# Optimization experiments

Hardware: AMD Instinct MI355X
Metric: run time of the kernel (lower is better)

The kernel has to match this reference:

```python
import jax, jax.numpy as jnp
import numpy as np

C = 256          # channels
H = 8            # attn heads
DH = C // H      # head dim
G = 2048         # number of graphs
NPG = 100        # nodes per graph
N = G * NPG      # total nodes
EPS = 1e-5       # batchnorm eps


def setup_inputs() -> dict:
    key = jax.random.key(0)
    ks = jax.random.split(key, 14)
    std = 0.02
    inp = {
        "x0": jax.random.normal(ks[0], (N, C), jnp.float32),
        "x1": jax.random.normal(ks[1], (N, C), jnp.float32),
        "batch": jnp.repeat(jnp.arange(G, dtype=jnp.int64), NPG)[:, None],
        # branch 0: linear + BN affine
        "p0_W": jax.random.normal(ks[2], (C, C), jnp.float32) * std,
        "p0_b": jnp.zeros((C,), jnp.float32),
        "p0_g": jnp.ones((C,), jnp.float32),
        "p0_beta": jnp.zeros((C,), jnp.float32),
        # branch 1
        "p1_W": jax.random.normal(ks[3], (C, C), jnp.float32) * std,
        "p1_b": jnp.zeros((C,), jnp.float32),
        "p1_g": jnp.ones((C,), jnp.float32),
        "p1_beta": jnp.zeros((C,), jnp.float32),
        # merge
        "merge_W": jax.random.normal(ks[4], (C, 2 * C), jnp.float32) * std,
        "merge_b": jnp.zeros((C,), jnp.float32),
        # MHA in_proj (packed q,k,v as in torch) and out_proj
        "in_proj_W": jax.random.normal(ks[5], (3 * C, C), jnp.float32) * std,
        "in_proj_b": jnp.zeros((3 * C,), jnp.float32),
        "out_proj_W": jax.random.normal(ks[6], (C, C), jnp.float32) * std,
        "out_proj_b": jnp.zeros((C,), jnp.float32),
        # readout
        "readout_W": jax.random.normal(ks[7], (1, C), jnp.float32) * std,
        "readout_b": jnp.zeros((1,), jnp.float32),
    }
    return inp


def _lin_bn_relu(x, W, b, g, beta):
    y = x @ W.T + b
    mu = jnp.mean(y, axis=0)
    var = jnp.var(y, axis=0)  # biased, matches torch BN training normalization
    return jax.nn.relu((y - mu) * jax.lax.rsqrt(var + EPS) * g + beta)


def reference(x0, x1, batch,
              p0_W, p0_b, p0_g, p0_beta,
              p1_W, p1_b, p1_g, p1_beta,
              merge_W, merge_b,
              in_proj_W, in_proj_b,
              out_proj_W, out_proj_b,
              readout_W, readout_b):
    seg = batch[:, 0]                                   # [N] sorted graph ids
    h0 = _lin_bn_relu(x0, p0_W, p0_b, p0_g, p0_beta)
    h1 = _lin_bn_relu(x1, p1_W, p1_b, p1_g, p1_beta)
    x = jnp.concatenate([h0, h1], axis=1) @ merge_W.T + merge_b  # [N,C]

    Wq, Wk, Wv = jnp.split(in_proj_W, 3, axis=0)
    bq, bk, bv = jnp.split(in_proj_b, 3, axis=0)
    # query is all-ones (length-1 sequence), shared across graphs
    q = (jnp.ones((C,), x.dtype) @ Wq.T + bq).reshape(H, DH) / jnp.sqrt(jnp.float32(DH))
    k = (x @ Wk.T + bk).reshape(-1, H, DH)              # [N,H,dh]
    v = (x @ Wv.T + bv).reshape(-1, H, DH)              # [N,H,dh]

    scores = jnp.einsum('hd,nhd->nh', q, k)            # [N,H]
    # segmented softmax over nodes of each graph
    m = jax.ops.segment_max(scores, seg, num_segments=G)      # [G,H]
    e = jnp.exp(scores - m[seg])                               # [N,H]
    denom = jax.ops.segment_sum(e, seg, num_segments=G)       # [G,H]
    pooled = jax.ops.segment_sum(e[:, :, None] * v, seg, num_segments=G)  # [G,H,dh]
    pooled = pooled / denom[:, :, None]

    attn = pooled.reshape(G, C) @ out_proj_W.T + out_proj_b   # [G,C]
    out = jnp.tanh(attn @ readout_W.T + readout_b)            # [G,1]
    return out
```

## Files before the change

kernel.cpp:

```cpp
#include <hip/hip_runtime.h>
#include <stdint.h>

#define NROWS 204800
#define NBLK_Y 1600
#define GRP 2048
#define NPG 100

typedef __attribute__((ext_vector_type(4))) float f32x4;
typedef __attribute__((ext_vector_type(8))) short bf16x8;
typedef __attribute__((ext_vector_type(4))) short bf16x4;

__device__ __forceinline__ unsigned bcu(float f){ union{float f;unsigned u;}c; c.f=f; return c.u; }
__device__ __forceinline__ float bcf(unsigned u){ union{unsigned u;float f;}c; c.u=u; return c.f; }
__device__ __forceinline__ short f2bf_rne(float f){ unsigned u=bcu(f); unsigned r=(u+0x7fffu+((u>>16)&1u))>>16; return (short)r; }
__device__ __forceinline__ unsigned pk_trunc(float lo, float hi){
  return __builtin_amdgcn_perm(bcu(hi), bcu(lo), 0x07060302u);
}
__device__ __forceinline__ f32x4 mfma16(bf16x8 a, bf16x8 b, f32x4 c){
  return __builtin_amdgcn_mfma_f32_16x16x32_bf16(a, b, c, 0, 0, 0);
}
#define BFLY16(v) { v += __shfl_xor(v,1); v += __shfl_xor(v,2); v += __shfl_xor(v,4); v += __shfl_xor(v,8); }

__global__ void k_cast_w(const float* __restrict__ w0, const float* __restrict__ w1,
                         short* __restrict__ out){
  int t = blockIdx.x*256 + threadIdx.x;
  const float* src = (t < 16384) ? w0 : w1;
  int base = (t & 16383) * 4;
  f32x4 v = *(const f32x4*)(src + base);
  bf16x4 o; o[0]=f2bf_rne(v[0]); o[1]=f2bf_rne(v[1]); o[2]=f2bf_rne(v[2]); o[3]=f2bf_rne(v[3]);
  *(bf16x4*)(out + ((t<16384)?0:65536) + base) = o;
}

__global__ void __launch_bounds__(256, 2)
k_gemm_y(const float* __restrict__ x0, const float* __restrict__ x1,
         const short* __restrict__ Wb,
         const float* __restrict__ b0p, const float* __restrict__ b1p,
         short* __restrict__ y0, short* __restrict__ y1,
         float* __restrict__ stats){
  __shared__ float st_sh[4][256][2];
  int bid = blockIdx.x;
  int which = (bid >= NBLK_Y) ? 1 : 0;
  const float* __restrict__ X = which ? x1 : x0;
  short* __restrict__ Y = which ? y1 : y0;
  const short* __restrict__ W = Wb + which*65536;
  const float* __restrict__ bias = which ? b1p : b0p;
  int n0 = (which ? bid - NBLK_Y : bid) * 128;
  int t = threadIdx.x, lane = t & 63, w = t >> 6;
  int l15 = lane & 15, q = lane >> 4;

  f32x4 acc[16][2];
  #pragma unroll
  for (int mt=0; mt<16; mt++){ acc[mt][0] = f32x4{0,0,0,0}; acc[mt][1] = f32x4{0,0,0,0}; }

  int nb = n0 + w*32;
  const float* xr0 = X + (nb + l15)*256;
  const float* xr1 = X + (nb + 16 + l15)*256;
  const short* wrow = W + l15*256;

  for (int ks=0; ks<8; ks++){
    int kq = ks*32 + q*8;
    f32x4 xa0 = *(const f32x4*)(xr0 + kq);
    f32x4 xb0 = *(const f32x4*)(xr0 + kq + 4);
    f32x4 xa1 = *(const f32x4*)(xr1 + kq);
    f32x4 xb1 = *(const f32x4*)(xr1 + kq + 4);
    int4 p0; p0.x=(int)pk_trunc(xa0[0],xa0[1]); p0.y=(int)pk_trunc(xa0[2],xa0[3]);
             p0.z=(int)pk_trunc(xb0[0],xb0[1]); p0.w=(int)pk_trunc(xb0[2],xb0[3]);
    int4 p1; p1.x=(int)pk_trunc(xa1[0],xa1[1]); p1.y=(int)pk_trunc(xa1[2],xa1[3]);
             p1.z=(int)pk_trunc(xb1[0],xb1[1]); p1.w=(int)pk_trunc(xb1[2],xb1[3]);
    bf16x8 bf0 = __builtin_bit_cast(bf16x8, p0);
    bf16x8 bf1 = __builtin_bit_cast(bf16x8, p1);
    #pragma unroll
    for (int mt=0; mt<16; mt++){
      bf16x8 af = *(const bf16x8*)(wrow + mt*4096 + kq);
      acc[mt][0] = mfma16(af, bf0, acc[mt][0]);
      acc[mt][1] = mfma16(af, bf1, acc[mt][1]);
    }
  }

  short* yo0 = Y + (nb + l15)*256 + q*4;
  short* yo1 = Y + (nb + 16 + l15)*256 + q*4;
  #pragma unroll
  for (int mt=0; mt<16; mt++){
    f32x4 bb = *(const f32x4*)(bias + mt*16 + q*4);
    f32x4 v0 = acc[mt][0] + bb;
    f32x4 v1 = acc[mt][1] + bb;
    int2 s0v; s0v.x=(int)pk_trunc(v0[0],v0[1]); s0v.y=(int)pk_trunc(v0[2],v0[3]);
    *(int2*)(yo0 + mt*16) = s0v;
    int2 s1v; s1v.x=(int)pk_trunc(v1[0],v1[1]); s1v.y=(int)pk_trunc(v1[2],v1[3]);
    *(int2*)(yo1 + mt*16) = s1v;
    float sa0=v0[0]+v1[0], sa1=v0[1]+v1[1], sa2=v0[2]+v1[2], sa3=v0[3]+v1[3];
    float qa0=v0[0]*v0[0]+v1[0]*v1[0], qa1=v0[1]*v0[1]+v1[1]*v1[1];
    float qa2=v0[2]*v0[2]+v1[2]*v1[2], qa3=v0[3]*v0[3]+v1[3]*v1[3];
    BFLY16(sa0); BFLY16(sa1); BFLY16(sa2); BFLY16(sa3);
    BFLY16(qa0); BFLY16(qa1); BFLY16(qa2); BFLY16(qa3);
    if (l15 == 0){
      int c0 = mt*16 + q*4;
      st_sh[w][c0+0][0]=sa0; st_sh[w][c0+0][1]=qa0;
      st_sh[w][c0+1][0]=sa1; st_sh[w][c0+1][1]=qa1;
      st_sh[w][c0+2][0]=sa2; st_sh[w][c0+2][1]=qa2;
      st_sh[w][c0+3][0]=sa3; st_sh[w][c0+3][1]=qa3;
    }
  }
  __syncthreads();
  {
    float ss = st_sh[0][t][0]+st_sh[1][t][0]+st_sh[2][t][0]+st_sh[3][t][0];
    float qq = st_sh[0][t][1]+st_sh[1][t][1]+st_sh[2][t][1]+st_sh[3][t][1];
    int rep = bid & 7;
    atomicAdd(&stats[rep*1024 + which*512 + t], ss);
    atomicAdd(&stats[rep*1024 + which*512 + 256 + t], qq);
  }
}

__global__ void k_small(const float* __restrict__ inW, const float* __restrict__ inB,
                        const float* __restrict__ mergeB,
                        const float* __restrict__ g0, const float* __restrict__ be0,
                        const float* __restrict__ g1, const float* __restrict__ be1,
                        const float* __restrict__ outW, const float* __restrict__ outB,
                        const float* __restrict__ rout, const float* __restrict__ routB,
                        const float* __restrict__ stats,
                        float* __restrict__ prm, float* __restrict__ qk){
  __shared__ float qv_sh[256], ck_sh[256];
  int t = threadIdx.x;
  const float invN = 1.0f/(float)NROWS;
  float s0=0, sq0=0, s1=0, sq1=0;
  for (int r=0;r<8;r++){
    s0  += stats[r*1024 + t];       sq0 += stats[r*1024 + 256 + t];
    s1  += stats[r*1024 + 512 + t]; sq1 += stats[r*1024 + 768 + t];
  }
  {
    float mu = s0*invN, var = sq0*invN - mu*mu;
    float rs = rsqrtf(var + 1e-5f);
    float a = g0[t]*rs;
    prm[t] = a; prm[512+t] = be0[t] - mu*a;
  }
  {
    float mu = s1*invN, var = sq1*invN - mu*mu;
    float rs = rsqrtf(var + 1e-5f);
    float a = g1[t]*rs;
    prm[256+t] = a; prm[768+t] = be1[t] - mu*a;
  }
  float qs = inB[t];
  for (int k=0;k<256;k++) qs += inW[t*256 + k];
  qv_sh[t] = qs * 0.17677669529663689f;
  float cks = inB[256+t];
  for (int m=0;m<256;m++) cks += mergeB[m] * inW[(256+t)*256 + m];
  ck_sh[t] = cks;
  float cvs = inB[512+t];
  for (int m=0;m<256;m++) cvs += mergeB[m] * inW[(512+t)*256 + m];
  prm[1024+t] = cvs;
  float wf = 0;
  for (int m=0;m<256;m++) wf += rout[m] * outW[m*256 + t];
  prm[1288+t] = wf;
  __syncthreads();
  for (int r=0;r<8;r++){
    int idx = r*256 + t; int h = idx>>8, m = idx&255;
    float s = 0;
    for (int d=0;d<32;d++) s += qv_sh[h*32+d] * inW[(256 + h*32 + d)*256 + m];
    qk[h*256+m] = s;
  }
  if (t < 8){
    float cs_ = 0;
    for (int d=0;d<32;d++) cs_ += qv_sh[t*32+d]*ck_sh[t*32+d];
    prm[1280+t] = cs_;
  }
  if (t == 0){
    float cf = routB[0];
    for (int m=0;m<256;m++) cf += rout[m]*outB[m];
    prm[1544] = cf;
  }
}

__global__ void k_wall(const float* __restrict__ inW, const float* __restrict__ mergeW,
                       const float* __restrict__ qk, short* __restrict__ Wall){
  int c = blockIdx.x; int t = threadIdx.x;
  if (c >= 264){
    Wall[c*512 + t] = 0; Wall[c*512 + 256 + t] = 0; return;
  }
  const float* src = (c < 256) ? (inW + (512+c)*256) : (qk + (c-256)*256);
  float a0=0, a1=0;
  for (int m=0;m<256;m++){
    float wm = src[m];
    a0 += wm * mergeW[m*512 + t];
    a1 += wm * mergeW[m*512 + 256 + t];
  }
  Wall[c*512 + t]       = f2bf_rne(a0);
  Wall[c*512 + 256 + t] = f2bf_rne(a1);
}

__global__ void __launch_bounds__(256, 2)
k_fused(const short* __restrict__ y0, const short* __restrict__ y1,
        const short* __restrict__ Wall, const float* __restrict__ prm,
        float* __restrict__ num, float* __restrict__ den){
  __shared__ float a_sh[512], b_sh[512], cv_sh[256], cs_sh[8];
  int t = threadIdx.x, lane = t & 63, w = t >> 6;
  int l15 = lane & 15, q = lane >> 4;
  for (int i=t; i<512; i+=256){ a_sh[i] = prm[i]; b_sh[i] = prm[512+i]; }
  cv_sh[t] = prm[1024+t];
  if (t < 8) cs_sh[t] = prm[1280+t];
  __syncthreads();

  int n0 = blockIdx.x*128, nb = n0 + w*32;
  f32x4 acc[17][2];
  #pragma unroll
  for (int mt=0; mt<17; mt++){ acc[mt][0] = f32x4{0,0,0,0}; acc[mt][1] = f32x4{0,0,0,0}; }

  for (int ks=0; ks<16; ks++){
    int jq = ks*32 + q*8;
    const short* ybase = (ks < 8) ? y0 : y1;
    int jj = jq & 255;
    f32x4 paL = *(const f32x4*)&a_sh[jq];  f32x4 paH = *(const f32x4*)&a_sh[jq+4];
    f32x4 pbL = *(const f32x4*)&b_sh[jq];  f32x4 pbH = *(const f32x4*)&b_sh[jq+4];
    bf16x8 bfr[2];
    #pragma unroll
    for (int nt=0; nt<2; nt++){
      int4 raw = *(const int4*)(ybase + (nb + nt*16 + l15)*256 + jj);
      unsigned r0=(unsigned)raw.x, r1=(unsigned)raw.y, r2=(unsigned)raw.z, r3=(unsigned)raw.w;
      float h0 = fmaxf(fmaf(bcf(r0<<16),         paL[0], pbL[0]), 0.f);
      float h1 = fmaxf(fmaf(bcf(r0&0xffff0000u), paL[1], pbL[1]), 0.f);
      float h2 = fmaxf(fmaf(bcf(r1<<16),         paL[2], pbL[2]), 0.f);
      float h3 = fmaxf(fmaf(bcf(r1&0xffff0000u), paL[3], pbL[3]), 0.f);
      float h4 = fmaxf(fmaf(bcf(r2<<16),         paH[0], pbH[0]), 0.f);
      float h5 = fmaxf(fmaf(bcf(r2&0xffff0000u), paH[1], pbH[1]), 0.f);
      float h6 = fmaxf(fmaf(bcf(r3<<16),         paH[2], pbH[2]), 0.f);
      float h7 = fmaxf(fmaf(bcf(r3&0xffff0000u), paH[3], pbH[3]), 0.f);
      int4 pk; pk.x=(int)pk_trunc(h0,h1); pk.y=(int)pk_trunc(h2,h3);
               pk.z=(int)pk_trunc(h4,h5); pk.w=(int)pk_trunc(h6,h7);
      bfr[nt] = __builtin_bit_cast(bf16x8, pk);
    }
    const short* wbase = Wall + l15*512 + jq;
    #pragma unroll
    for (int mt=0; mt<17; mt++){
      bf16x8 af = *(const bf16x8*)(wbase + mt*8192);
      acc[mt][0] = mfma16(af, bfr[0], acc[mt][0]);
      acc[mt][1] = mfma16(af, bfr[1], acc[mt][1]);
    }
  }

  float e0[4], e1[4];
  #pragma unroll
  for (int i=0;i<4;i++){
    float cadd = (q<2) ? cs_sh[q*4+i] : 0.f;
    e0[i] = (q<2) ? __expf(acc[16][0][i] + cadd) : 0.f;
    e1[i] = (q<2) ? __expf(acc[16][1][i] + cadd) : 0.f;
  }
  #pragma unroll
  for (int nt=0; nt<2; nt++){
    int tb = nb + nt*16;
    int sg = tb/100; int brow = (sg+1)*100 - tb; bool split = brow < 16;
    float d0[4], d1[4];
    #pragma unroll
    for (int i=0;i<4;i++){
      float ev = nt ? e1[i] : e0[i];
      d0[i] = (l15 < brow) ? ev : 0.f; d1[i] = ev - d0[i];
    }
    BFLY16(d0[0]); BFLY16(d0[1]); BFLY16(d0[2]); BFLY16(d0[3]);
    if (split){ BFLY16(d1[0]); BFLY16(d1[1]); BFLY16(d1[2]); BFLY16(d1[3]); }
    if (l15==0 && q<2){
      #pragma unroll
      for (int i=0;i<4;i++) atomicAdd(&den[sg*8 + q*4 + i], d0[i]);
      if (split){
        #pragma unroll
        for (int i=0;i<4;i++) atomicAdd(&den[(sg+1)*8 + q*4 + i], d1[i]);
      }
    }
  }
  #pragma unroll
  for (int mt=0; mt<16; mt++){
    const int h = mt>>1, hq = h>>2, hi = h&3;
    f32x4 cvv = *(const f32x4*)&cv_sh[mt*16 + q*4];
    #pragma unroll
    for (int nt=0; nt<2; nt++){
      float esrc = nt ? e1[hi] : e0[hi];
      float eb = __shfl(esrc, hq*16 + l15, 64);
      int tb = nb + nt*16;
      int sg = tb/100; int brow = (sg+1)*100 - tb; bool split = brow < 16;
      float p0[4], p1[4];
      #pragma unroll
      for (int i=0;i<4;i++){
        float wv = (acc[mt][nt][i] + cvv[i]) * eb;
        p0[i] = (l15 < brow) ? wv : 0.f; p1[i] = wv - p0[i];
      }
      BFLY16(p0[0]); BFLY16(p0[1]); BFLY16(p0[2]); BFLY16(p0[3]);
      if (split){ BFLY16(p1[0]); BFLY16(p1[1]); BFLY16(p1[2]); BFLY16(p1[3]); }
      if (l15==0){
        int c0 = mt*16 + q*4;
        #pragma unroll
        for (int i=0;i<4;i++) atomicAdd(&num[sg*256 + c0 + i], p0[i]);
        if (split){
          #pragma unroll
          for (int i=0;i<4;i++) atomicAdd(&num[(sg+1)*256 + c0 + i], p1[i]);
        }
      }
    }
  }
}

__global__ void k_out(const float* __restrict__ num, const float* __restrict__ den,
                      const float* __restrict__ prm, float* __restrict__ out){
  int g = blockIdx.x; int lane = threadIdx.x;
  f32x4 nm = *(const f32x4*)(num + g*256 + lane*4);
  f32x4 wf = *(const f32x4*)(prm + 1288 + lane*4);
  float dh = den[g*8 + (lane>>3)];
  float v = (nm[0]*wf[0] + nm[1]*wf[1] + nm[2]*wf[2] + nm[3]*wf[3]) / dh;
  v += __shfl_xor(v,1); v += __shfl_xor(v,2); v += __shfl_xor(v,4);
  v += __shfl_xor(v,8); v += __shfl_xor(v,16); v += __shfl_xor(v,32);
  if (lane==0) out[g] = tanhf(v + prm[1544]);
}

extern "C" void kernel_launch(void* const* d_in, const int* in_sizes, int n_in,
                              void* d_out, int out_size, void* d_ws, size_t ws_size,
                              hipStream_t stream){
  const float* x0      = (const float*)d_in[0];
  const float* x1      = (const float*)d_in[1];
  const float* p0_W    = (const float*)d_in[3];
  const float* p0_b    = (const float*)d_in[4];
  const float* p0_g    = (const float*)d_in[5];
  const float* p0_beta = (const float*)d_in[6];
  const float* p1_W    = (const float*)d_in[7];
  const float* p1_b    = (const float*)d_in[8];
  const float* p1_g    = (const float*)d_in[9];
  const float* p1_beta = (const float*)d_in[10];
  const float* merge_W = (const float*)d_in[11];
  const float* merge_b = (const float*)d_in[12];
  const float* inp_W   = (const float*)d_in[13];
  const float* inp_b   = (const float*)d_in[14];
  const float* out_W   = (const float*)d_in[15];
  const float* out_b   = (const float*)d_in[16];
  const float* ro_W    = (const float*)d_in[17];
  const float* ro_b    = (const float*)d_in[18];
  float* outp = (float*)d_out;

  char* ws = (char*)d_ws;
  short* y0w   = (short*)(ws);
  short* y1w   = (short*)(ws + 104857600);
  short* Wb    = (short*)(ws + 209715200);
  short* Wall  = (short*)(ws + 209977344);
  float* stats = (float*)(ws + 210255872);
  float* num   = (float*)(ws + 210288640);
  float* den   = (float*)(ws + 212385792);
  float* prm   = (float*)(ws + 212451328);
  float* qk    = (float*)(ws + 212459520);

  hipMemsetAsync(ws + 210255872, 0, 2195456, stream);

  k_cast_w<<<dim3(128), dim3(256), 0, stream>>>(p0_W, p1_W, Wb);
  k_gemm_y<<<dim3(2*NBLK_Y), dim3(256), 0, stream>>>(x0, x1, Wb, p0_b, p1_b, y0w, y1w, stats);
  k_small<<<dim3(1), dim3(256), 0, stream>>>(inp_W, inp_b, merge_b, p0_g, p0_beta, p1_g, p1_beta,
                                             out_W, out_b, ro_W, ro_b, stats, prm, qk);
  k_wall<<<dim3(272), dim3(256), 0, stream>>>(inp_W, merge_W, qk, Wall);
  k_fused<<<dim3(NBLK_Y), dim3(256), 0, stream>>>(y0w, y1w, Wall, prm, num, den);
  k_out<<<dim3(GRP), dim3(64), 0, stream>>>(num, den, prm, outp);
}
```

Measured before the change: 1.017 ms.

## Restructure GEMMs to keep activations in registers and stream weight tiles per output block

Both the first GEMM and the fused merge/KV kernel now load and convert the whole activation strip into registers up front. They then loop over output column tiles, computing each tile's full K reduction with double-buffered weight fragment loads. This replaces the large per-thread accumulator array with two accumulators, which frees registers; the first kernel's launch bounds are raised to allow 3 blocks per CU. The epilogue work (softmax denominators, weighted num atomics) is interleaved per tile, with the score tile computed first. Register pressure from the held activations and weights may still limit occupancy or cause spills.

```diff
diff --git a/kernel.cpp b/kernel.cpp
--- a/kernel.cpp
+++ b/kernel.cpp
@@ -31,7 +31,7 @@
   *(bf16x4*)(out + ((t<16384)?0:65536) + base) = o;
 }
 
-__global__ void __launch_bounds__(256, 2)
+__global__ void __launch_bounds__(256, 3)
 k_gemm_y(const float* __restrict__ x0, const float* __restrict__ x1,
          const short* __restrict__ Wb,
          const float* __restrict__ b0p, const float* __restrict__ b1p,
@@ -47,43 +47,57 @@
   int n0 = (which ? bid - NBLK_Y : bid) * 128;
   int t = threadIdx.x, lane = t & 63, w = t >> 6;
   int l15 = lane & 15, q = lane >> 4;
-
-  f32x4 acc[16][2];
-  #pragma unroll
-  for (int mt=0; mt<16; mt++){ acc[mt][0] = f32x4{0,0,0,0}; acc[mt][1] = f32x4{0,0,0,0}; }
-
   int nb = n0 + w*32;
-  const float* xr0 = X + (nb + l15)*256;
-  const float* xr1 = X + (nb + 16 + l15)*256;
+
   const short* wrow = W + l15*256;
 
-  for (int ks=0; ks<8; ks++){
-    int kq = ks*32 + q*8;
-    f32x4 xa0 = *(const f32x4*)(xr0 + kq);
-    f32x4 xb0 = *(const f32x4*)(xr0 + kq + 4);
-    f32x4 xa1 = *(const f32x4*)(xr1 + kq);
-    f32x4 xb1 = *(const f32x4*)(xr1 + kq + 4);
-    int4 p0; p0.x=(int)pk_trunc(xa0[0],xa0[1]); p0.y=(int)pk_trunc(xa0[2],xa0[3]);
-             p0.z=(int)pk_trunc(xb0[0],xb0[1]); p0.w=(int)pk_trunc(xb0[2],xb0[3]);
-    int4 p1; p1.x=(int)pk_trunc(xa1[0],xa1[1]); p1.y=(int)pk_trunc(xa1[2],xa1[3]);
-             p1.z=(int)pk_trunc(xb1[0],xb1[1]); p1.w=(int)pk_trunc(xb1[2],xb1[3]);
-    bf16x8 bf0 = __builtin_bit_cast(bf16x8, p0);
-    bf16x8 bf1 = __builtin_bit_cast(bf16x8, p1);
-    #pragma unroll
-    for (int mt=0; mt<16; mt++){
-      bf16x8 af = *(const bf16x8*)(wrow + mt*4096 + kq);
-      acc[mt][0] = mfma16(af, bf0, acc[mt][0]);
-      acc[mt][1] = mfma16(af, bf1, acc[mt][1]);
+  bf16x8 wfA[4], wfB[4];
+  #pragma unroll
+  for (int ks=0; ks<4; ks++)
+    wfA[ks] = *(const bf16x8*)(wrow + ks*32 + q*8);
+
+  bf16x8 xb[2][8];
+  #pragma unroll
+  for (int g=0; g<2; g++){
+    const float* xr = X + (nb + g*16 + l15)*256;
+    #pragma unroll
+    for (int ks=0; ks<8; ks++){
+      int kq = ks*32 + q*8;
+      f32x4 a = *(const f32x4*)(xr + kq);
+      f32x4 b = *(const f32x4*)(xr + kq + 4);
+      int4 p; p.x=(int)pk_trunc(a[0],a[1]); p.y=(int)pk_trunc(a[2],a[3]);
+              p.z=(int)pk_trunc(b[0],b[1]); p.w=(int)pk_trunc(b[2],b[3]);
+      xb[g][ks] = __builtin_bit_cast(bf16x8, p);
     }
   }
 
   short* yo0 = Y + (nb + l15)*256 + q*4;
   short* yo1 = Y + (nb + 16 + l15)*256 + q*4;
+
   #pragma unroll
   for (int mt=0; mt<16; mt++){
+    #pragma unroll
+    for (int ks=0; ks<4; ks++)
+      wfB[ks] = *(const bf16x8*)(wrow + mt*4096 + (ks+4)*32 + q*8);
+    f32x4 acc0 = f32x4{0,0,0,0}, acc1 = f32x4{0,0,0,0};
+    #pragma unroll
+    for (int ks=0; ks<4; ks++){
+      acc0 = mfma16(wfA[ks], xb[0][ks], acc0);
+      acc1 = mfma16(wfA[ks], xb[1][ks], acc1);
+    }
+    if (mt < 15){
+      #pragma unroll
+      for (int ks=0; ks<4; ks++)
+        wfA[ks] = *(const bf16x8*)(wrow + (mt+1)*4096 + ks*32 + q*8);
+    }
+    #pragma unroll
+    for (int ks=0; ks<4; ks++){
+      acc0 = mfma16(wfB[ks], xb[0][ks+4], acc0);
+      acc1 = mfma16(wfB[ks], xb[1][ks+4], acc1);
+    }
     f32x4 bb = *(const f32x4*)(bias + mt*16 + q*4);
-    f32x4 v0 = acc[mt][0] + bb;
-    f32x4 v1 = acc[mt][1] + bb;
+    f32x4 v0 = acc0 + bb;
+    f32x4 v1 = acc1 + bb;
     int2 s0v; s0v.x=(int)pk_trunc(v0[0],v0[1]); s0v.y=(int)pk_trunc(v0[2],v0[3]);
     *(int2*)(yo0 + mt*16) = s0v;
     int2 s1v; s1v.x=(int)pk_trunc(v1[0],v1[1]); s1v.y=(int)pk_trunc(v1[2],v1[3]);
@@ -200,20 +214,24 @@
   __syncthreads();
 
   int n0 = blockIdx.x*128, nb = n0 + w*32;
-  f32x4 acc[17][2];
-  #pragma unroll
-  for (int mt=0; mt<17; mt++){ acc[mt][0] = f32x4{0,0,0,0}; acc[mt][1] = f32x4{0,0,0,0}; }
-
+  const short* wbase = Wall + l15*512;
+
+  bf16x8 wfA[8], wfB[8];
+  #pragma unroll
+  for (int ks=0; ks<8; ks++)
+    wfA[ks] = *(const bf16x8*)(wbase + 16*8192 + ks*32 + q*8);
+
+  bf16x8 xb[2][16];
+  #pragma unroll
   for (int ks=0; ks<16; ks++){
     int jq = ks*32 + q*8;
     const short* ybase = (ks < 8) ? y0 : y1;
     int jj = jq & 255;
     f32x4 paL = *(const f32x4*)&a_sh[jq];  f32x4 paH = *(const f32x4*)&a_sh[jq+4];
     f32x4 pbL = *(const f32x4*)&b_sh[jq];  f32x4 pbH = *(const f32x4*)&b_sh[jq+4];
-    bf16x8 bfr[2];
-    #pragma unroll
-    for (int nt=0; nt<2; nt++){
-      int4 raw = *(const int4*)(ybase + (nb + nt*16 + l15)*256 + jj);
+    #pragma unroll
+    for (int g=0; g<2; g++){
+      int4 raw = *(const int4*)(ybase + (nb + g*16 + l15)*256 + jj);
       unsigned r0=(unsigned)raw.x, r1=(unsigned)raw.y, r2=(unsigned)raw.z, r3=(unsigned)raw.w;
       float h0 = fmaxf(fmaf(bcf(r0<<16),         paL[0], pbL[0]), 0.f);
       float h1 = fmaxf(fmaf(bcf(r0&0xffff0000u), paL[1], pbL[1]), 0.f);
@@ -225,70 +243,89 @@
       float h7 = fmaxf(fmaf(bcf(r3&0xffff0000u), paH[3], pbH[3]), 0.f);
       int4 pk; pk.x=(int)pk_trunc(h0,h1); pk.y=(int)pk_trunc(h2,h3);
                pk.z=(int)pk_trunc(h4,h5); pk.w=(int)pk_trunc(h6,h7);
-      bfr[nt] = __builtin_bit_cast(bf16x8, pk);
-    }
-    const short* wbase = Wall + l15*512 + jq;
-    #pragma unroll
-    for (int mt=0; mt<17; mt++){
-      bf16x8 af = *(const bf16x8*)(wbase + mt*8192);
-      acc[mt][0] = mfma16(af, bfr[0], acc[mt][0]);
-      acc[mt][1] = mfma16(af, bfr[1], acc[mt][1]);
+      xb[g][ks] = __builtin_bit_cast(bf16x8, pk);
     }
   }
 
   float e0[4], e1[4];
-  #pragma unroll
-  for (int i=0;i<4;i++){
-    float cadd = (q<2) ? cs_sh[q*4+i] : 0.f;
-    e0[i] = (q<2) ? __expf(acc[16][0][i] + cadd) : 0.f;
-    e1[i] = (q<2) ? __expf(acc[16][1][i] + cadd) : 0.f;
-  }
-  #pragma unroll
-  for (int nt=0; nt<2; nt++){
-    int tb = nb + nt*16;
-    int sg = tb/100; int brow = (sg+1)*100 - tb; bool split = brow < 16;
-    float d0[4], d1[4];
-    #pragma unroll
-    for (int i=0;i<4;i++){
-      float ev = nt ? e1[i] : e0[i];
-      d0[i] = (l15 < brow) ? ev : 0.f; d1[i] = ev - d0[i];
-    }
-    BFLY16(d0[0]); BFLY16(d0[1]); BFLY16(d0[2]); BFLY16(d0[3]);
-    if (split){ BFLY16(d1[0]); BFLY16(d1[1]); BFLY16(d1[2]); BFLY16(d1[3]); }
-    if (l15==0 && q<2){
-      #pragma unroll
-      for (int i=0;i<4;i++) atomicAdd(&den[sg*8 + q*4 + i], d0[i]);
-      if (split){
+
+  #pragma unroll
+  for (int idx=0; idx<17; idx++){
+    const int T = (idx==0) ? 16 : (idx-1);
+    #pragma unroll
+    for (int ks=0; ks<8; ks++)
+      wfB[ks] = *(const bf16x8*)(wbase + T*8192 + (ks+8)*32 + q*8);
+    f32x4 acc0 = f32x4{0,0,0,0}, acc1 = f32x4{0,0,0,0};
+    #pragma unroll
+    for (int ks=0; ks<8; ks++){
+      acc0 = mfma16(wfA[ks], xb[0][ks], acc0);
+      acc1 = mfma16(wfA[ks], xb[1][ks], acc1);
+    }
+    if (idx < 16){
+      #pragma unroll
+      for (int ks=0; ks<8; ks++)
+        wfA[ks] = *(const bf16x8*)(wbase + idx*8192 + ks*32 + q*8);
+    }
+    #pragma unroll
+    for (int ks=0; ks<8; ks++){
+      acc0 = mfma16(wfB[ks], xb[0][ks+8], acc0);
+      acc1 = mfma16(wfB[ks], xb[1][ks+8], acc1);
+    }
+
+    if (T == 16){
+      #pragma unroll
+      for (int i=0;i<4;i++){
+        float cadd = (q<2) ? cs_sh[q*4+i] : 0.f;
+        e0[i] = (q<2) ? __expf(acc0[i] + cadd) : 0.f;
+        e1[i] = (q<2) ? __expf(acc1[i] + cadd) : 0.f;
+      }
+      #pragma unroll
+      for (int nt=0; nt<2; nt++){
+        int tb = nb + nt*16;
+        int sg = tb/100; int brow = (sg+1)*100 - tb; bool split = brow < 16;
+        float d0[4], d1[4];
         #pragma unroll
-        for (int i=0;i<4;i++) atomicAdd(&den[(sg+1)*8 + q*4 + i], d1[i]);
+        for (int i=0;i<4;i++){
+          float ev = nt ? e1[i] : e0[i];
+          d0[i] = (l15 < brow) ? ev : 0.f; d1[i] = ev - d0[i];
+        }
+        BFLY16(d0[0]); BFLY16(d0[1]); BFLY16(d0[2]); BFLY16(d0[3]);
+        if (split){ BFLY16(d1[0]); BFLY16(d1[1]); BFLY16(d1[2]); BFLY16(d1[3]); }
+        if (l15==0 && q<2){
+          #pragma unroll
+          for (int i=0;i<4;i++) atomicAdd(&den[sg*8 + q*4 + i], d0[i]);
+          if (split){
+            #pragma unroll
+            for (int i=0;i<4;i++) atomicAdd(&den[(sg+1)*8 + q*4 + i], d1[i]);
+          }
+        }
       }
-    }
-  }
-  #pragma unroll
-  for (int mt=0; mt<16; mt++){
-    const int h = mt>>1, hq = h>>2, hi = h&3;
-    f32x4 cvv = *(const f32x4*)&cv_sh[mt*16 + q*4];
-    #pragma unroll
-    for (int nt=0; nt<2; nt++){
-      float esrc = nt ? e1[hi] : e0[hi];
-      float eb = __shfl(esrc, hq*16 + l15, 64);
-      int tb = nb + nt*16;
-      int sg = tb/100; int brow = (sg+1)*100 - tb; bool split = brow < 16;
-      float p0[4], p1[4];
-      #pragma unroll
-      for (int i=0;i<4;i++){
-        float wv = (acc[mt][nt][i] + cvv[i]) * eb;
-        p0[i] = (l15 < brow) ? wv : 0.f; p1[i] = wv - p0[i];
-      }
-      BFLY16(p0[0]); BFLY16(p0[1]); BFLY16(p0[2]); BFLY16(p0[3]);
-      if (split){ BFLY16(p1[0]); BFLY16(p1[1]); BFLY16(p1[2]); BFLY16(p1[3]); }
-      if (l15==0){
-        int c0 = mt*16 + q*4;
+    } else {
+      const int h = T>>1, hq = h>>2, hi = h&3;
+      f32x4 cvv = *(const f32x4*)&cv_sh[T*16 + q*4];
+      #pragma unroll
+      for (int nt=0; nt<2; nt++){
+        float esrc = nt ? e1[hi] : e0[hi];
+        float eb = __shfl(esrc, hq*16 + l15, 64);
+        int tb = nb + nt*16;
+        int sg = tb/100; int brow = (sg+1)*100 - tb; bool split = brow < 16;
+        f32x4 accg = nt ? acc1 : acc0;
+        float p0[4], p1[4];
         #pragma unroll
-        for (int i=0;i<4;i++) atomicAdd(&num[sg*256 + c0 + i], p0[i]);
-        if (split){
+        for (int i=0;i<4;i++){
+          float wv = (accg[i] + cvv[i]) * eb;
+          p0[i] = (l15 < brow) ? wv : 0.f; p1[i] = wv - p0[i];
+        }
+        BFLY16(p0[0]); BFLY16(p0[1]); BFLY16(p0[2]); BFLY16(p0[3]);
+        if (split){ BFLY16(p1[0]); BFLY16(p1[1]); BFLY16(p1[2]); BFLY16(p1[3]); }
+        if (l15==0){
+          int c0 = T*16 + q*4;
           #pragma unroll
-          for (int i=0;i<4;i++) atomicAdd(&num[(sg+1)*256 + c0 + i], p1[i]);
+          for (int i=0;i<4;i++) atomicAdd(&num[sg*256 + c0 + i], p0[i]);
+          if (split){
+            #pragma unroll
+            for (int i=0;i<4;i++) atomicAdd(&num[(sg+1)*256 + c0 + i], p1[i]);
+          }
         }
       }
     }
```

Result: faster. 972.8 us (-4.4%).

## Stage GEMM operands through swizzled LDS with double-buffered async global-to-LDS loads

Applied to the files above, without the earlier changes.

Both main GEMM kernels now stage their X/y and weight tiles into shared memory using global_load_lds with an XOR swizzle, double-buffering the K loop so the next stage loads while MFMAs run on the current one. Weights are pre-laid-out in the swizzled order by k_cast_w and k_wall. k_fused moves to 512-thread blocks covering 256 rows, which halves the grid and shares the weight tile across more rows. The large LDS footprint (about 132 KB in k_fused) limits how many blocks fit per CU, and the extra barriers add sync cost.

```diff
diff --git a/kernel.cpp b/kernel.cpp
--- a/kernel.cpp
+++ b/kernel.cpp
@@ -3,12 +3,11 @@
 
 #define NROWS 204800
 #define NBLK_Y 1600
+#define NBLK_F 800
 #define GRP 2048
-#define NPG 100
 
 typedef __attribute__((ext_vector_type(4))) float f32x4;
 typedef __attribute__((ext_vector_type(8))) short bf16x8;
-typedef __attribute__((ext_vector_type(4))) short bf16x4;
 
 __device__ __forceinline__ unsigned bcu(float f){ union{float f;unsigned u;}c; c.f=f; return c.u; }
 __device__ __forceinline__ float bcf(unsigned u){ union{unsigned u;float f;}c; c.u=u; return c.f; }
@@ -19,66 +18,105 @@
 __device__ __forceinline__ f32x4 mfma16(bf16x8 a, bf16x8 b, f32x4 c){
   return __builtin_amdgcn_mfma_f32_16x16x32_bf16(a, b, c, 0, 0, 0);
 }
+__device__ __forceinline__ void gl16(const void* g, void* l){
+  __builtin_amdgcn_global_load_lds(
+      (const __attribute__((address_space(1))) void*)g,
+      (__attribute__((address_space(3))) void*)l, 16, 0, 0);
+}
 #define BFLY16(v) { v += __shfl_xor(v,1); v += __shfl_xor(v,2); v += __shfl_xor(v,4); v += __shfl_xor(v,8); }
 
 __global__ void k_cast_w(const float* __restrict__ w0, const float* __restrict__ w1,
                          short* __restrict__ out){
-  int t = blockIdx.x*256 + threadIdx.x;
-  const float* src = (t < 16384) ? w0 : w1;
-  int base = (t & 16383) * 4;
-  f32x4 v = *(const f32x4*)(src + base);
-  bf16x4 o; o[0]=f2bf_rne(v[0]); o[1]=f2bf_rne(v[1]); o[2]=f2bf_rne(v[2]); o[3]=f2bf_rne(v[3]);
-  *(bf16x4*)(out + ((t<16384)?0:65536) + base) = o;
-}
-
-__global__ void __launch_bounds__(256, 2)
+  int g = blockIdx.x*256 + threadIdx.x;
+  int which = g >> 13, r = g & 8191;
+  int col = r >> 5, s = (r >> 2) & 7, q = r & 3;
+  const float* src = (which ? w1 : w0) + col*256 + s*32 + q*8;
+  f32x4 a = *(const f32x4*)src;
+  f32x4 b = *(const f32x4*)(src + 4);
+  bf16x8 o;
+  o[0]=f2bf_rne(a[0]); o[1]=f2bf_rne(a[1]); o[2]=f2bf_rne(a[2]); o[3]=f2bf_rne(a[3]);
+  o[4]=f2bf_rne(b[0]); o[5]=f2bf_rne(b[1]); o[6]=f2bf_rne(b[2]); o[7]=f2bf_rne(b[3]);
+  int lu = ((col>>1)<<3) + ((((col&1)<<2) | q) ^ (col&7));
+  *(bf16x8*)(out + which*65536 + s*8192 + lu*8) = o;
+}
+
+__global__ void __launch_bounds__(256)
 k_gemm_y(const float* __restrict__ x0, const float* __restrict__ x1,
          const short* __restrict__ Wb,
          const float* __restrict__ b0p, const float* __restrict__ b1p,
          short* __restrict__ y0, short* __restrict__ y1,
          float* __restrict__ stats){
+  __shared__ __align__(16) char lds[65536];
   __shared__ float st_sh[4][256][2];
   int bid = blockIdx.x;
   int which = (bid >= NBLK_Y) ? 1 : 0;
   const float* __restrict__ X = which ? x1 : x0;
   short* __restrict__ Y = which ? y1 : y0;
-  const short* __restrict__ W = Wb + which*65536;
   const float* __restrict__ bias = which ? b1p : b0p;
   int n0 = (which ? bid - NBLK_Y : bid) * 128;
   int t = threadIdx.x, lane = t & 63, w = t >> 6;
   int l15 = lane & 15, q = lane >> 4;
+  const char* Wg = (const char*)Wb + (size_t)which*131072;
 
   f32x4 acc[16][2];
   #pragma unroll
-  for (int mt=0; mt<16; mt++){ acc[mt][0] = f32x4{0,0,0,0}; acc[mt][1] = f32x4{0,0,0,0}; }
-
-  int nb = n0 + w*32;
-  const float* xr0 = X + (nb + l15)*256;
-  const float* xr1 = X + (nb + 16 + l15)*256;
-  const short* wrow = W + l15*256;
-
-  for (int ks=0; ks<8; ks++){
-    int kq = ks*32 + q*8;
-    f32x4 xa0 = *(const f32x4*)(xr0 + kq);
-    f32x4 xb0 = *(const f32x4*)(xr0 + kq + 4);
-    f32x4 xa1 = *(const f32x4*)(xr1 + kq);
-    f32x4 xb1 = *(const f32x4*)(xr1 + kq + 4);
-    int4 p0; p0.x=(int)pk_trunc(xa0[0],xa0[1]); p0.y=(int)pk_trunc(xa0[2],xa0[3]);
-             p0.z=(int)pk_trunc(xb0[0],xb0[1]); p0.w=(int)pk_trunc(xb0[2],xb0[3]);
-    int4 p1; p1.x=(int)pk_trunc(xa1[0],xa1[1]); p1.y=(int)pk_trunc(xa1[2],xa1[3]);
-             p1.z=(int)pk_trunc(xb1[0],xb1[1]); p1.w=(int)pk_trunc(xb1[2],xb1[3]);
-    bf16x8 bf0 = __builtin_bit_cast(bf16x8, p0);
-    bf16x8 bf1 = __builtin_bit_cast(bf16x8, p1);
+  for (int mt=0; mt<16; mt++){ acc[mt][0]=f32x4{0,0,0,0}; acc[mt][1]=f32x4{0,0,0,0}; }
+
+  auto stage = [&](int s_, int b_){
+    #pragma unroll
+    for (int i=0;i<4;i++){
+      int uu = i*256 + t, row = uu>>3, cu = uu&7;
+      gl16((const char*)X + ((size_t)(n0+row)<<10) + (s_<<7) + ((cu ^ (row&7))<<4),
+           lds + b_*16384 + ((i*256 + (w<<6))<<4));
+    }
+    #pragma unroll
+    for (int i=0;i<4;i++)
+      gl16(Wg + (s_<<14) + ((i*256 + t)<<4),
+           lds + 32768 + b_*16384 + ((i*256 + (w<<6))<<4));
+  };
+
+  auto kstep = [&](int b_){
+    int swz = (l15&7)<<4;
+    bf16x8 hx0, hx1;
+    {
+      const char* p = lds + b_*16384;
+      int rowl = (w<<5) + l15;
+      f32x4 f0 = *(const f32x4*)(p + (((rowl<<7) + (q<<5)) ^ swz));
+      f32x4 f1 = *(const f32x4*)(p + (((rowl<<7) + (q<<5) + 16) ^ swz));
+      int4 pk4; pk4.x=(int)pk_trunc(f0[0],f0[1]); pk4.y=(int)pk_trunc(f0[2],f0[3]);
+                pk4.z=(int)pk_trunc(f1[0],f1[1]); pk4.w=(int)pk_trunc(f1[2],f1[3]);
+      hx0 = __builtin_bit_cast(bf16x8, pk4);
+      rowl += 16;
+      f32x4 g0 = *(const f32x4*)(p + (((rowl<<7) + (q<<5)) ^ swz));
+      f32x4 g1 = *(const f32x4*)(p + (((rowl<<7) + (q<<5) + 16) ^ swz));
+      pk4.x=(int)pk_trunc(g0[0],g0[1]); pk4.y=(int)pk_trunc(g0[2],g0[3]);
+      pk4.z=(int)pk_trunc(g1[0],g1[1]); pk4.w=(int)pk_trunc(g1[2],g1[3]);
+      hx1 = __builtin_bit_cast(bf16x8, pk4);
+    }
+    const char* wp = lds + 32768 + b_*16384;
     #pragma unroll
     for (int mt=0; mt<16; mt++){
-      bf16x8 af = *(const bf16x8*)(wrow + mt*4096 + kq);
-      acc[mt][0] = mfma16(af, bf0, acc[mt][0]);
-      acc[mt][1] = mfma16(af, bf1, acc[mt][1]);
-    }
-  }
-
-  short* yo0 = Y + (nb + l15)*256 + q*4;
-  short* yo1 = Y + (nb + 16 + l15)*256 + q*4;
+      int col = (mt<<4) + l15;
+      bf16x8 wf = *(const bf16x8*)(wp + (((col<<6) + (q<<4)) ^ swz));
+      acc[mt][0] = mfma16(wf, hx0, acc[mt][0]);
+      acc[mt][1] = mfma16(wf, hx1, acc[mt][1]);
+    }
+  };
+
+  stage(0, 0);
+  __syncthreads();
+  int buf = 0;
+  #pragma unroll
+  for (int s=0; s<8; s++){
+    if (s < 7) stage(s+1, buf^1);
+    kstep(buf);
+    __syncthreads();
+    buf ^= 1;
+  }
+
+  int nb = n0 + (w<<5);
+  short* yo0 = Y + (size_t)(nb + l15)*256 + q*4;
+  short* yo1 = yo0 + 16*256;
   #pragma unroll
   for (int mt=0; mt<16; mt++){
     f32x4 bb = *(const f32x4*)(bias + mt*16 + q*4);
@@ -173,75 +211,121 @@
 __global__ void k_wall(const float* __restrict__ inW, const float* __restrict__ mergeW,
                        const float* __restrict__ qk, short* __restrict__ Wall){
   int c = blockIdx.x; int t = threadIdx.x;
-  if (c >= 264){
-    Wall[c*512 + t] = 0; Wall[c*512 + 256 + t] = 0; return;
-  }
-  const float* src = (c < 256) ? (inW + (512+c)*256) : (qk + (c-256)*256);
-  float a0=0, a1=0;
-  for (int m=0;m<256;m++){
-    float wm = src[m];
-    a0 += wm * mergeW[m*512 + t];
-    a1 += wm * mergeW[m*512 + 256 + t];
-  }
-  Wall[c*512 + t]       = f2bf_rne(a0);
-  Wall[c*512 + 256 + t] = f2bf_rne(a1);
-}
-
-__global__ void __launch_bounds__(256, 2)
+  float a0 = 0.f, a1 = 0.f;
+  if (c < 264){
+    const float* src = (c < 256) ? (inW + (512+c)*256) : (qk + (c-256)*256);
+    for (int m=0;m<256;m++){
+      float wm = src[m];
+      a0 += wm * mergeW[m*512 + t];
+      a1 += wm * mergeW[m*512 + 256 + t];
+    }
+  }
+  int c7 = c & 7;
+  int u1 = (t>>3) & 7, e1 = t & 7;
+  int s1 = t >> 6;
+  Wall[s1*17408 + (c*8 + (u1 ^ c7))*8 + e1] = f2bf_rne(a0);
+  int s2 = 4 + (t >> 6);
+  Wall[s2*17408 + (c*8 + (u1 ^ c7))*8 + e1] = f2bf_rne(a1);
+}
+
+__global__ void __launch_bounds__(512)
 k_fused(const short* __restrict__ y0, const short* __restrict__ y1,
         const short* __restrict__ Wall, const float* __restrict__ prm,
         float* __restrict__ num, float* __restrict__ den){
-  __shared__ float a_sh[512], b_sh[512], cv_sh[256], cs_sh[8];
+  __shared__ __align__(16) char lds[135168];
   int t = threadIdx.x, lane = t & 63, w = t >> 6;
   int l15 = lane & 15, q = lane >> 4;
-  for (int i=t; i<512; i+=256){ a_sh[i] = prm[i]; b_sh[i] = prm[512+i]; }
-  cv_sh[t] = prm[1024+t];
-  if (t < 8) cs_sh[t] = prm[1280+t];
+  int gn0 = blockIdx.x << 8;
+  int row0 = t >> 3, cu = t & 7;
+
+  f32x4 acc[17][2];
+  #pragma unroll
+  for (int mt=0; mt<17; mt++){ acc[mt][0]=f32x4{0,0,0,0}; acc[mt][1]=f32x4{0,0,0,0}; }
+
+  int4 yr0, yr1, yr2, yr3;
+  f32x4 ca0, ca1, cb0, cb1;
+
+  auto fload = [&](int s_){
+    const short* ysel = (s_ < 4) ? y0 : y1;
+    int kb = (s_ & 3) << 6;
+    const short* rp = ysel + (size_t)(gn0 + row0)*256 + kb + (cu<<3);
+    yr0 = *(const int4*)(rp);
+    yr1 = *(const int4*)(rp +  64*256);
+    yr2 = *(const int4*)(rp + 128*256);
+    yr3 = *(const int4*)(rp + 192*256);
+    int j = (s_<<6) + (cu<<3);
+    ca0 = *(const f32x4*)(prm + j);        ca1 = *(const f32x4*)(prm + j + 4);
+    cb0 = *(const f32x4*)(prm + 512 + j);  cb1 = *(const f32x4*)(prm + 512 + j + 4);
+  };
+  auto fwall = [&](int s_, int b_){
+    const char* wg = (const char*)Wall + s_*34816;
+    char* ld = lds + 65536 + b_*34816;
+    #pragma unroll
+    for (int i=0;i<4;i++)
+      gl16(wg + ((i*512 + t)<<4), ld + ((i*512 + (w<<6))<<4));
+    if (w < 2)
+      gl16(wg + ((2048 + t)<<4), ld + ((2048 + (w<<6))<<4));
+  };
+  auto fwrite = [&](int b_){
+    #pragma unroll
+    for (int i=0;i<4;i++){
+      int4 raw = (i==0)?yr0 : (i==1)?yr1 : (i==2)?yr2 : yr3;
+      int row = (i<<6) + row0;
+      unsigned r0=(unsigned)raw.x, r1=(unsigned)raw.y, r2=(unsigned)raw.z, r3=(unsigned)raw.w;
+      float h0 = fmaxf(fmaf(bcf(r0<<16),         ca0[0], cb0[0]), 0.f);
+      float h1 = fmaxf(fmaf(bcf(r0&0xffff0000u), ca0[1], cb0[1]), 0.f);
+      float h2 = fmaxf(fmaf(bcf(r1<<16),         ca0[2], cb0[2]), 0.f);
+      float h3 = fmaxf(fmaf(bcf(r1&0xffff0000u), ca0[3], cb0[3]), 0.f);
+      float h4 = fmaxf(fmaf(bcf(r2<<16),         ca1[0], cb1[0]), 0.f);
+      float h5 = fmaxf(fmaf(bcf(r2&0xffff0000u), ca1[1], cb1[1]), 0.f);
+      float h6 = fmaxf(fmaf(bcf(r3<<16),         ca1[2], cb1[2]), 0.f);
+      float h7 = fmaxf(fmaf(bcf(r3&0xffff0000u), ca1[3], cb1[3]), 0.f);
+      int4 pk4; pk4.x=(int)pk_trunc(h0,h1); pk4.y=(int)pk_trunc(h2,h3);
+                pk4.z=(int)pk_trunc(h4,h5); pk4.w=(int)pk_trunc(h6,h7);
+      *(int4*)(lds + b_*32768 + (row<<7) + ((cu ^ (row&7))<<4)) = pk4;
+    }
+  };
+  auto kstep = [&](int b_){
+    int swz = (l15&7)<<4;
+    #pragma unroll
+    for (int ksub=0; ksub<2; ksub++){
+      int ko = ((ksub<<2) + q) << 4;
+      bf16x8 hx0, hx1;
+      {
+        int rowl = (w<<5) + l15;
+        hx0 = *(const bf16x8*)(lds + b_*32768 + (((rowl<<7) + ko) ^ swz));
+        hx1 = *(const bf16x8*)(lds + b_*32768 + ((((rowl+16)<<7) + ko) ^ swz));
+      }
+      const char* wp = lds + 65536 + b_*34816;
+      #pragma unroll
+      for (int mt=0; mt<17; mt++){
+        int col = (mt<<4) + l15;
+        bf16x8 wf = *(const bf16x8*)(wp + (((col<<7) + ko) ^ swz));
+        acc[mt][0] = mfma16(wf, hx0, acc[mt][0]);
+        acc[mt][1] = mfma16(wf, hx1, acc[mt][1]);
+      }
+    }
+  };
+
+  fload(0); fwall(0, 0); fwrite(0);
   __syncthreads();
-
-  int n0 = blockIdx.x*128, nb = n0 + w*32;
-  f32x4 acc[17][2];
-  #pragma unroll
-  for (int mt=0; mt<17; mt++){ acc[mt][0] = f32x4{0,0,0,0}; acc[mt][1] = f32x4{0,0,0,0}; }
-
-  for (int ks=0; ks<16; ks++){
-    int jq = ks*32 + q*8;
-    const short* ybase = (ks < 8) ? y0 : y1;
-    int jj = jq & 255;
-    f32x4 paL = *(const f32x4*)&a_sh[jq];  f32x4 paH = *(const f32x4*)&a_sh[jq+4];
-    f32x4 pbL = *(const f32x4*)&b_sh[jq];  f32x4 pbH = *(const f32x4*)&b_sh[jq+4];
-    bf16x8 bfr[2];
-    #pragma unroll
-    for (int nt=0; nt<2; nt++){
-      int4 raw = *(const int4*)(ybase + (nb + nt*16 + l15)*256 + jj);
-      unsigned r0=(unsigned)raw.x, r1=(unsigned)raw.y, r2=(unsigned)raw.z, r3=(unsigned)raw.w;
-      float h0 = fmaxf(fmaf(bcf(r0<<16),         paL[0], pbL[0]), 0.f);
-      float h1 = fmaxf(fmaf(bcf(r0&0xffff0000u), paL[1], pbL[1]), 0.f);
-      float h2 = fmaxf(fmaf(bcf(r1<<16),         paL[2], pbL[2]), 0.f);
-      float h3 = fmaxf(fmaf(bcf(r1&0xffff0000u), paL[3], pbL[3]), 0.f);
-      float h4 = fmaxf(fmaf(bcf(r2<<16),         paH[0], pbH[0]), 0.f);
-      float h5 = fmaxf(fmaf(bcf(r2&0xffff0000u), paH[1], pbH[1]), 0.f);
-      float h6 = fmaxf(fmaf(bcf(r3<<16),         paH[2], pbH[2]), 0.f);
-      float h7 = fmaxf(fmaf(bcf(r3&0xffff0000u), paH[3], pbH[3]), 0.f);
-      int4 pk; pk.x=(int)pk_trunc(h0,h1); pk.y=(int)pk_trunc(h2,h3);
-               pk.z=(int)pk_trunc(h4,h5); pk.w=(int)pk_trunc(h6,h7);
-      bfr[nt] = __builtin_bit_cast(bf16x8, pk);
-    }
-    const short* wbase = Wall + l15*512 + jq;
-    #pragma unroll
-    for (int mt=0; mt<17; mt++){
-      bf16x8 af = *(const bf16x8*)(wbase + mt*8192);
-      acc[mt][0] = mfma16(af, bfr[0], acc[mt][0]);
-      acc[mt][1] = mfma16(af, bfr[1], acc[mt][1]);
-    }
-  }
-
+  int buf = 0;
+  #pragma unroll
+  for (int s=0; s<8; s++){
+    if (s < 7){ fload(s+1); fwall(s+1, buf^1); }
+    kstep(buf);
+    if (s < 7) fwrite(buf^1);
+    __syncthreads();
+    buf ^= 1;
+  }
+
+  int nb = gn0 + (w<<5);
+  f32x4 csv = *(const f32x4*)(prm + 1280 + q*4);
   float e0[4], e1[4];
   #pragma unroll
   for (int i=0;i<4;i++){
-    float cadd = (q<2) ? cs_sh[q*4+i] : 0.f;
-    e0[i] = (q<2) ? __expf(acc[16][0][i] + cadd) : 0.f;
-    e1[i] = (q<2) ? __expf(acc[16][1][i] + cadd) : 0.f;
+    e0[i] = (q<2) ? __expf(acc[16][0][i] + csv[i]) : 0.f;
+    e1[i] = (q<2) ? __expf(acc[16][1][i] + csv[i]) : 0.f;
   }
   #pragma unroll
   for (int nt=0; nt<2; nt++){
@@ -267,17 +351,18 @@
   #pragma unroll
   for (int mt=0; mt<16; mt++){
     const int h = mt>>1, hq = h>>2, hi = h&3;
-    f32x4 cvv = *(const f32x4*)&cv_sh[mt*16 + q*4];
+    f32x4 cvv = *(const f32x4*)(prm + 1024 + mt*16 + q*4);
     #pragma unroll
     for (int nt=0; nt<2; nt++){
       float esrc = nt ? e1[hi] : e0[hi];
       float eb = __shfl(esrc, hq*16 + l15, 64);
       int tb = nb + nt*16;
       int sg = tb/100; int brow = (sg+1)*100 - tb; bool split = brow < 16;
+      f32x4 accg = acc[mt][nt];
       float p0[4], p1[4];
       #pragma unroll
       for (int i=0;i<4;i++){
-        float wv = (acc[mt][nt][i] + cvv[i]) * eb;
+        float wv = (accg[i] + cvv[i]) * eb;
         p0[i] = (l15 < brow) ? wv : 0.f; p1[i] = wv - p0[i];
       }
       BFLY16(p0[0]); BFLY16(p0[1]); BFLY16(p0[2]); BFLY16(p0[3]);
@@ -343,11 +428,11 @@
 
   hipMemsetAsync(ws + 210255872, 0, 2195456, stream);
 
-  k_cast_w<<<dim3(128), dim3(256), 0, stream>>>(p0_W, p1_W, Wb);
+  k_cast_w<<<dim3(64), dim3(256), 0, stream>>>(p0_W, p1_W, Wb);
   k_gemm_y<<<dim3(2*NBLK_Y), dim3(256), 0, stream>>>(x0, x1, Wb, p0_b, p1_b, y0w, y1w, stats);
   k_small<<<dim3(1), dim3(256), 0, stream>>>(inp_W, inp_b, merge_b, p0_g, p0_beta, p1_g, p1_beta,
                                              out_W, out_b, ro_W, ro_b, stats, prm, qk);
   k_wall<<<dim3(272), dim3(256), 0, stream>>>(inp_W, merge_W, qk, Wall);
-  k_fused<<<dim3(NBLK_Y), dim3(256), 0, stream>>>(y0w, y1w, Wall, prm, num, den);
+  k_fused<<<dim3(NBLK_F), dim3(512), 0, stream>>>(y0w, y1w, Wall, prm, num, den);
   k_out<<<dim3(GRP), dim3(64), 0, stream>>>(num, den, prm, outp);
 }
```

New measurement: 961.9 us. 1.06x faster.
